# Optimization experiments

Hardware: AMD Instinct MI355X
Metric: run time of the kernel (lower is better)

## Reference

```python
import jax, jax.numpy as jnp
import numpy as np

B = 131072   # batch of states (e.g. ODE integrator batch)
S = 2        # state_dim (q, p)
H = 512      # hidden_dim
E = 8        # action_embedding_dim


def setup_inputs() -> dict:
    key = jax.random.key(0)
    ks = jax.random.split(key, 8)
    sc = lambda n: 1.0 / np.sqrt(n)
    return {
        "t": 0,  # unused time scalar (odeint signature)
        "state": jax.random.normal(ks[0], (B, S), dtype=jnp.float32),
        "action_emb": jax.random.normal(ks[1], (B, E), dtype=jnp.float32),
        # H_net: Linear(S,H) -> Softplus -> Linear(H,H) -> Softplus -> Linear(H,1)
        "W1": jax.random.normal(ks[2], (S, H), dtype=jnp.float32) * sc(S),
        "b1": jnp.zeros((H,), dtype=jnp.float32),
        "W2": jax.random.normal(ks[3], (H, H), dtype=jnp.float32) * sc(H),
        "b2": jnp.zeros((H,), dtype=jnp.float32),
        "W3": jax.random.normal(ks[4], (H, 1), dtype=jnp.float32) * sc(H),
        "b3": jnp.zeros((1,), dtype=jnp.float32),
        "log_damping": jnp.asarray(-1.0, dtype=jnp.float32),
        # G_net: Linear(E, S//2)
        "Gw": jax.random.normal(ks[5], (E, S // 2), dtype=jnp.float32) * sc(E),
        "Gb": jnp.zeros((S // 2,), dtype=jnp.float32),
    }


def reference(t, state, action_emb, W1, b1, W2, b2, W3, b3, log_damping, Gw, Gb):
    # Hamiltonian net: scalar H per state; sum over batch so jax.grad gives
    # per-sample dH/dstate in one pass (equivalent to autograd.grad with ones cotangent).
    def H_sum(s):
        h = jax.nn.softplus(s @ W1 + b1)       # [B, H]
        h = jax.nn.softplus(h @ W2 + b2)       # [B, H]
        return jnp.sum(h @ W3 + b3)            # scalar

    dH_dstate = jax.grad(H_sum)(state)         # [B, S]
    dH_dq = dH_dstate[..., 0:1]                # [B, 1]
    dH_dp = dH_dstate[..., 1:2]                # [B, 1]

    damping = jnp.exp(log_damping)
    G_u = action_emb @ Gw + Gb                 # [B, 1]

    dq_dt = dH_dp
    dp_dt = -dH_dq - damping * dH_dp + G_u
    return jnp.concatenate([dq_dt, dp_dt], axis=-1)  # [B, S]
```

## Files before the change

### kernel.cpp

```cpp
#include <hip/hip_runtime.h>

typedef __bf16 bf16x8 __attribute__((ext_vector_type(8)));
typedef float f32x4 __attribute__((ext_vector_type(4)));
typedef unsigned short u16x8 __attribute__((ext_vector_type(8)));

#define DEVI static __device__ __forceinline__

DEVI unsigned short f2b(float x) {
  __bf16 b = (__bf16)x;
  return __builtin_bit_cast(unsigned short, b);
}

__global__ __launch_bounds__(256) void pack_w2_kernel(
    const float* __restrict__ W2, unsigned short* __restrict__ p1,
    unsigned short* __restrict__ p2) {
  int idx = blockIdx.x * 256 + threadIdx.x;
  int which = idx >> 18;
  int i = idx & 262143;
  int j = i & 7;
  int l = (i >> 3) & 63;
  int t0 = (i >> 9) & 31;
  int t1 = i >> 14;
  if (which == 0) {
    p1[i] = f2b(W2[(t1 * 32 + (l >> 4) * 8 + j) * 512 + t0 * 16 + (l & 15)]);
  } else {
    p2[i] = f2b(W2[(t0 * 16 + (l & 15)) * 512 + t1 * 32 + (l >> 4) * 8 + j]);
  }
}

__global__ __launch_bounds__(256, 2) void phm_kernel(
    const float* __restrict__ state, const float* __restrict__ action_emb,
    const float* __restrict__ W1, const float* __restrict__ b1,
    const float* __restrict__ b2, const float* __restrict__ W3,
    const float* __restrict__ log_damping, const float* __restrict__ Gw,
    const float* __restrict__ Gb, const unsigned short* __restrict__ packB1,
    const unsigned short* __restrict__ packB2, float* __restrict__ out) {
  __shared__ unsigned short buf[64 * 512];
  __shared__ float W1s[1024];
  __shared__ float b1s[512];
  __shared__ float b2s[512];
  __shared__ float W3s[512];
  __shared__ float st[128];
  __shared__ float part[4][64][2];

  const int t = threadIdx.x;
  const int lane = t & 63;
  const int wid = t >> 6;
  const int l15 = lane & 15;
  const int l4 = lane >> 4;
  const long row0 = (long)blockIdx.x * 64;
  const f32x4 fzero = {0.f, 0.f, 0.f, 0.f};

  for (int i = t; i < 512; i += 256) {
    W1s[i] = W1[i];
    W1s[512 + i] = W1[512 + i];
    b1s[i] = b1[i];
    b2s[i] = b2[i];
    W3s[i] = W3[i];
  }
  if (t < 128) st[t] = state[row0 * 2 + t];
  __syncthreads();

  for (int it = 0; it < 16; ++it) {
    int gid = it * 256 + t;
    int r = gid >> 6;
    int cg = gid & 63;
    float s0 = st[r * 2], s1 = st[r * 2 + 1];
    u16x8 pk;
#pragma unroll
    for (int j = 0; j < 8; ++j) {
      int c = cg * 8 + j;
      float z = fmaf(s0, W1s[c], fmaf(s1, W1s[512 + c], b1s[c]));
      float e = __expf(-fabsf(z));
      float h = fmaxf(z, 0.f) + __logf(1.f + e);
      pk[j] = f2b(h);
    }
    int bo = (cg * 16) ^ ((r & 15) << 4);
    *reinterpret_cast<u16x8*>(reinterpret_cast<char*>(buf) + r * 1024 + bo) = pk;
  }
  __syncthreads();

  f32x4 acc1[2][4][4];
#pragma unroll
  for (int ch = 0; ch < 2; ++ch)
#pragma unroll
    for (int a = 0; a < 4; ++a)
#pragma unroll
      for (int b = 0; b < 4; ++b) acc1[ch][a][b] = fzero;

#pragma unroll
  for (int chunk = 0; chunk < 2; ++chunk) {
    const int c0 = wid * 128 + chunk * 64;
#pragma unroll 2
    for (int kt = 0; kt < 16; ++kt) {
      bf16x8 af[4];
      int bo = (kt * 64 + l4 * 16) ^ (l15 << 4);
#pragma unroll
      for (int rt = 0; rt < 4; ++rt) {
        int rr = rt * 16 + l15;
        af[rt] = __builtin_bit_cast(
            bf16x8, *reinterpret_cast<const int4*>(
                        reinterpret_cast<const char*>(buf) + rr * 1024 + bo));
      }
      bf16x8 bfr[4];
#pragma unroll
      for (int ct = 0; ct < 4; ++ct) {
        int frag = kt * 32 + (c0 >> 4) + ct;
        bfr[ct] = __builtin_bit_cast(
            bf16x8,
            *reinterpret_cast<const int4*>(packB1 + (frag * 64 + lane) * 8));
      }
#pragma unroll
      for (int rt = 0; rt < 4; ++rt)
#pragma unroll
        for (int ct = 0; ct < 4; ++ct)
          acc1[chunk][rt][ct] = __builtin_amdgcn_mfma_f32_16x16x32_bf16(
              af[rt], bfr[ct], acc1[chunk][rt][ct], 0, 0, 0);
    }
  }
  __syncthreads();

#pragma unroll
  for (int chunk = 0; chunk < 2; ++chunk) {
    const int c0 = wid * 128 + chunk * 64;
#pragma unroll
    for (int ct = 0; ct < 4; ++ct) {
      int c = c0 + ct * 16 + l15;
      float w3 = W3s[c], bb = b2s[c];
#pragma unroll
      for (int rt = 0; rt < 4; ++rt) {
#pragma unroll
        for (int j = 0; j < 4; ++j) {
          int r = rt * 16 + l4 * 4 + j;
          float z2 = acc1[chunk][rt][ct][j] + bb;
          float sg = __builtin_amdgcn_rcpf(1.f + __expf(-z2));
          unsigned short u = f2b(w3 * sg);
          int bo = (c * 2) ^ ((r & 15) << 4);
          *reinterpret_cast<unsigned short*>(
              reinterpret_cast<char*>(buf) + r * 1024 + bo) = u;
        }
      }
    }
  }
  __syncthreads();

  float2 sv[16];
#pragma unroll
  for (int rt = 0; rt < 4; ++rt)
#pragma unroll
    for (int j = 0; j < 4; ++j) {
      int r = rt * 16 + l4 * 4 + j;
      sv[rt * 4 + j] = *reinterpret_cast<const float2*>(&st[r * 2]);
    }

  float p0[16], p1v[16];
#pragma unroll
  for (int i = 0; i < 16; ++i) { p0[i] = 0.f; p1v[i] = 0.f; }

  for (int chunk = 0; chunk < 2; ++chunk) {
    const int k0c = wid * 128 + chunk * 64;
    f32x4 acc[4][4];
#pragma unroll
    for (int a = 0; a < 4; ++a)
#pragma unroll
      for (int b = 0; b < 4; ++b) acc[a][b] = fzero;

#pragma unroll 2
    for (int ct2 = 0; ct2 < 16; ++ct2) {
      bf16x8 af[4];
      int bo = (ct2 * 64 + l4 * 16) ^ (l15 << 4);
#pragma unroll
      for (int rt = 0; rt < 4; ++rt) {
        int rr = rt * 16 + l15;
        af[rt] = __builtin_bit_cast(
            bf16x8, *reinterpret_cast<const int4*>(
                        reinterpret_cast<const char*>(buf) + rr * 1024 + bo));
      }
      bf16x8 bfr[4];
#pragma unroll
      for (int kt = 0; kt < 4; ++kt) {
        int frag = ct2 * 32 + (k0c >> 4) + kt;
        bfr[kt] = __builtin_bit_cast(
            bf16x8,
            *reinterpret_cast<const int4*>(packB2 + (frag * 64 + lane) * 8));
      }
#pragma unroll
      for (int rt = 0; rt < 4; ++rt)
#pragma unroll
        for (int kt = 0; kt < 4; ++kt)
          acc[rt][kt] = __builtin_amdgcn_mfma_f32_16x16x32_bf16(
              af[rt], bfr[kt], acc[rt][kt], 0, 0, 0);
    }
#pragma unroll
    for (int kt = 0; kt < 4; ++kt) {
      int kc = k0c + kt * 16 + l15;
      float w10 = W1s[kc], w11 = W1s[512 + kc], bb = b1s[kc];
#pragma unroll
      for (int rt = 0; rt < 4; ++rt) {
#pragma unroll
        for (int j = 0; j < 4; ++j) {
          float2 s = sv[rt * 4 + j];
          float z1 = fmaf(s.x, w10, fmaf(s.y, w11, bb));
          float sg = __builtin_amdgcn_rcpf(1.f + __expf(-z1));
          float dz1 = acc[rt][kt][j] * sg;
          p0[rt * 4 + j] = fmaf(dz1, w10, p0[rt * 4 + j]);
          p1v[rt * 4 + j] = fmaf(dz1, w11, p1v[rt * 4 + j]);
        }
      }
    }
  }

#pragma unroll
  for (int i = 0; i < 16; ++i) {
    float a = p0[i], b = p1v[i];
    for (int m = 1; m < 16; m <<= 1) {
      a += __shfl_xor(a, m, 64);
      b += __shfl_xor(b, m, 64);
    }
    p0[i] = a;
    p1v[i] = b;
  }
  if (l15 == 0) {
#pragma unroll
    for (int rt = 0; rt < 4; ++rt)
#pragma unroll
      for (int j = 0; j < 4; ++j) {
        int r = rt * 16 + l4 * 4 + j;
        part[wid][r][0] = p0[rt * 4 + j];
        part[wid][r][1] = p1v[rt * 4 + j];
      }
  }
  __syncthreads();

  if (t < 64) {
    long grow = row0 + t;
    float g0 = part[0][t][0] + part[1][t][0] + part[2][t][0] + part[3][t][0];
    float g1 = part[0][t][1] + part[1][t][1] + part[2][t][1] + part[3][t][1];
    const float4 ae0 = reinterpret_cast<const float4*>(action_emb)[grow * 2];
    const float4 ae1 = reinterpret_cast<const float4*>(action_emb)[grow * 2 + 1];
    float gu = Gb[0];
    gu = fmaf(ae0.x, Gw[0], gu);
    gu = fmaf(ae0.y, Gw[1], gu);
    gu = fmaf(ae0.z, Gw[2], gu);
    gu = fmaf(ae0.w, Gw[3], gu);
    gu = fmaf(ae1.x, Gw[4], gu);
    gu = fmaf(ae1.y, Gw[5], gu);
    gu = fmaf(ae1.z, Gw[6], gu);
    gu = fmaf(ae1.w, Gw[7], gu);
    float damping = __expf(log_damping[0]);
    float2 o;
    o.x = g1;
    o.y = -g0 - damping * g1 + gu;
    reinterpret_cast<float2*>(out)[grow] = o;
  }
}

extern "C" void kernel_launch(void* const* d_in, const int* in_sizes, int n_in,
                              void* d_out, int out_size, void* d_ws,
                              size_t ws_size, hipStream_t stream) {
  const float* state = (const float*)d_in[1];
  const float* action_emb = (const float*)d_in[2];
  const float* W1 = (const float*)d_in[3];
  const float* b1 = (const float*)d_in[4];
  const float* W2 = (const float*)d_in[5];
  const float* b2 = (const float*)d_in[6];
  const float* W3 = (const float*)d_in[7];
  const float* log_damping = (const float*)d_in[9];
  const float* Gw = (const float*)d_in[10];
  const float* Gb = (const float*)d_in[11];
  float* out = (float*)d_out;

  unsigned short* p1 = (unsigned short*)d_ws;
  unsigned short* p2 = p1 + 262144;

  pack_w2_kernel<<<dim3(2048), dim3(256), 0, stream>>>(W2, p1, p2);
  phm_kernel<<<dim3(2048), dim3(256), 0, stream>>>(
      state, action_emb, W1, b1, b2, W3, log_damping, Gw, Gb, p1, p2, out);
}
```

Before: 177.5 us.

## Use 32x32x16 MFMA for forward GEMM with fragment-ordered LDS layout

Switches the forward H@W2 GEMM from 16x16x32 to 32x32x16 bf16 MFMA tiles, with a matching repacking of W2. The first hidden activations are stored in LDS as pre-swizzled, fragment-contiguous pages, so each lane reads its operand with one linear 16-byte load. The backward GEMM is restructured to keep all 8 column tiles of 16x16 accumulators live in a single pass instead of two chunks. The intent is fewer MFMA issues, simpler LDS addressing and fewer repeated A-fragment loads. The trade-off is higher register pressure and more complex scatter writes for the sigmoid-gradient stage.

```diff
diff --git a/kernel.cpp b/kernel.cpp
--- a/kernel.cpp
+++ b/kernel.cpp
@@ -2,6 +2,7 @@
 
 typedef __bf16 bf16x8 __attribute__((ext_vector_type(8)));
 typedef float f32x4 __attribute__((ext_vector_type(4)));
+typedef float f32x16 __attribute__((ext_vector_type(16)));
 typedef unsigned short u16x8 __attribute__((ext_vector_type(8)));
 
 #define DEVI static __device__ __forceinline__
@@ -19,12 +20,14 @@
   int i = idx & 262143;
   int j = i & 7;
   int l = (i >> 3) & 63;
-  int t0 = (i >> 9) & 31;
-  int t1 = i >> 14;
   if (which == 0) {
-    p1[i] = f2b(W2[(t1 * 32 + (l >> 4) * 8 + j) * 512 + t0 * 16 + (l & 15)]);
+    int t0 = (i >> 9) & 15;
+    int s = i >> 13;
+    p1[i] = f2b(W2[(s * 16 + (l >> 5) * 8 + j) * 512 + t0 * 32 + (l & 31)]);
   } else {
-    p2[i] = f2b(W2[(t0 * 16 + (l & 15)) * 512 + t1 * 32 + (l >> 4) * 8 + j]);
+    int t0 = (i >> 9) & 31;
+    int s = i >> 14;
+    p2[i] = f2b(W2[(t0 * 16 + (l & 15)) * 512 + s * 32 + (l >> 4) * 8 + j]);
   }
 }
 
@@ -48,8 +51,10 @@
   const int wid = t >> 6;
   const int l15 = lane & 15;
   const int l4 = lane >> 4;
+  const int l31 = lane & 31;
+  const int l5 = lane >> 5;
   const long row0 = (long)blockIdx.x * 64;
-  const f32x4 fzero = {0.f, 0.f, 0.f, 0.f};
+  char* bufc = reinterpret_cast<char*>(buf);
 
   for (int i = t; i < 512; i += 256) {
     W1s[i] = W1[i];
@@ -62,150 +67,136 @@
   __syncthreads();
 
   for (int it = 0; it < 16; ++it) {
-    int gid = it * 256 + t;
-    int r = gid >> 6;
-    int cg = gid & 63;
-    float s0 = st[r * 2], s1 = st[r * 2 + 1];
+    int page = it * 4 + wid;
+    int s = page >> 1, rt = page & 1;
+    int row = rt * 32 + l31;
+    int k0 = s * 16 + l5 * 8;
+    float s0 = st[row * 2], s1 = st[row * 2 + 1];
     u16x8 pk;
 #pragma unroll
     for (int j = 0; j < 8; ++j) {
-      int c = cg * 8 + j;
+      int c = k0 + j;
       float z = fmaf(s0, W1s[c], fmaf(s1, W1s[512 + c], b1s[c]));
       float e = __expf(-fabsf(z));
       float h = fmaxf(z, 0.f) + __logf(1.f + e);
       pk[j] = f2b(h);
     }
-    int bo = (cg * 16) ^ ((r & 15) << 4);
-    *reinterpret_cast<u16x8*>(reinterpret_cast<char*>(buf) + r * 1024 + bo) = pk;
-  }
-  __syncthreads();
-
-  f32x4 acc1[2][4][4];
-#pragma unroll
-  for (int ch = 0; ch < 2; ++ch)
-#pragma unroll
-    for (int a = 0; a < 4; ++a)
-#pragma unroll
-      for (int b = 0; b < 4; ++b) acc1[ch][a][b] = fzero;
-
-#pragma unroll
-  for (int chunk = 0; chunk < 2; ++chunk) {
-    const int c0 = wid * 128 + chunk * 64;
+    *reinterpret_cast<u16x8*>(bufc + page * 1024 + lane * 16) = pk;
+  }
+  __syncthreads();
+
+  f32x16 acc1[2][4];
+#pragma unroll
+  for (int rt = 0; rt < 2; ++rt)
+#pragma unroll
+    for (int ct = 0; ct < 4; ++ct)
+#pragma unroll
+      for (int r = 0; r < 16; ++r) acc1[rt][ct][r] = 0.f;
+
+#pragma unroll 4
+  for (int s = 0; s < 32; ++s) {
+    bf16x8 af[2];
+#pragma unroll
+    for (int rt = 0; rt < 2; ++rt)
+      af[rt] = __builtin_bit_cast(
+          bf16x8, *reinterpret_cast<const int4*>(
+                      bufc + (s * 2 + rt) * 1024 + lane * 16));
+    bf16x8 bfr[4];
+#pragma unroll
+    for (int ct = 0; ct < 4; ++ct)
+      bfr[ct] = __builtin_bit_cast(
+          bf16x8, *reinterpret_cast<const int4*>(
+                      packB1 + ((s * 16 + wid * 4 + ct) * 64 + lane) * 8));
+#pragma unroll
+    for (int rt = 0; rt < 2; ++rt)
+#pragma unroll
+      for (int ct = 0; ct < 4; ++ct)
+        acc1[rt][ct] = __builtin_amdgcn_mfma_f32_32x32x16_bf16(
+            af[rt], bfr[ct], acc1[rt][ct], 0, 0, 0);
+  }
+  __syncthreads();
+
+#pragma unroll
+  for (int rt = 0; rt < 2; ++rt) {
+#pragma unroll
+    for (int ct = 0; ct < 4; ++ct) {
+      int c = wid * 128 + ct * 32 + l31;
+      float w3 = W3s[c], bb = b2s[c];
+      int pbase = (c >> 5) * 4096 + (c & 7) * 2;
+      int oct = (l31 >> 3);
+#pragma unroll
+      for (int reg = 0; reg < 16; ++reg) {
+        int row = rt * 32 + (reg & 3) + 8 * (reg >> 2) + 4 * l5;
+        float z2 = acc1[rt][ct][reg] + bb;
+        float sg = __builtin_amdgcn_rcpf(1.f + __expf(-z2));
+        unsigned short u = f2b(w3 * sg);
+        int lane2 = (row & 15) + 16 * oct;
+        int slot = lane2 ^ (lane2 >> 4);
+        *reinterpret_cast<unsigned short*>(
+            bufc + pbase + (row >> 4) * 1024 + slot * 16) = u;
+      }
+    }
+  }
+  __syncthreads();
+
+  float2 sv[16];
+#pragma unroll
+  for (int rt2 = 0; rt2 < 4; ++rt2)
+#pragma unroll
+    for (int jj = 0; jj < 4; ++jj) {
+      int r = rt2 * 16 + l4 * 4 + jj;
+      sv[rt2 * 4 + jj] = *reinterpret_cast<const float2*>(&st[r * 2]);
+    }
+
+  f32x4 acc2[4][8];
+#pragma unroll
+  for (int a = 0; a < 4; ++a)
+#pragma unroll
+    for (int b = 0; b < 8; ++b)
+#pragma unroll
+      for (int r = 0; r < 4; ++r) acc2[a][b][r] = 0.f;
+
+  const int rslot = (lane ^ (lane >> 4)) * 16;
 #pragma unroll 2
-    for (int kt = 0; kt < 16; ++kt) {
-      bf16x8 af[4];
-      int bo = (kt * 64 + l4 * 16) ^ (l15 << 4);
-#pragma unroll
-      for (int rt = 0; rt < 4; ++rt) {
-        int rr = rt * 16 + l15;
-        af[rt] = __builtin_bit_cast(
-            bf16x8, *reinterpret_cast<const int4*>(
-                        reinterpret_cast<const char*>(buf) + rr * 1024 + bo));
-      }
-      bf16x8 bfr[4];
-#pragma unroll
-      for (int ct = 0; ct < 4; ++ct) {
-        int frag = kt * 32 + (c0 >> 4) + ct;
-        bfr[ct] = __builtin_bit_cast(
-            bf16x8,
-            *reinterpret_cast<const int4*>(packB1 + (frag * 64 + lane) * 8));
-      }
-#pragma unroll
-      for (int rt = 0; rt < 4; ++rt)
-#pragma unroll
-        for (int ct = 0; ct < 4; ++ct)
-          acc1[chunk][rt][ct] = __builtin_amdgcn_mfma_f32_16x16x32_bf16(
-              af[rt], bfr[ct], acc1[chunk][rt][ct], 0, 0, 0);
-    }
-  }
-  __syncthreads();
-
-#pragma unroll
-  for (int chunk = 0; chunk < 2; ++chunk) {
-    const int c0 = wid * 128 + chunk * 64;
-#pragma unroll
-    for (int ct = 0; ct < 4; ++ct) {
-      int c = c0 + ct * 16 + l15;
-      float w3 = W3s[c], bb = b2s[c];
-#pragma unroll
-      for (int rt = 0; rt < 4; ++rt) {
-#pragma unroll
-        for (int j = 0; j < 4; ++j) {
-          int r = rt * 16 + l4 * 4 + j;
-          float z2 = acc1[chunk][rt][ct][j] + bb;
-          float sg = __builtin_amdgcn_rcpf(1.f + __expf(-z2));
-          unsigned short u = f2b(w3 * sg);
-          int bo = (c * 2) ^ ((r & 15) << 4);
-          *reinterpret_cast<unsigned short*>(
-              reinterpret_cast<char*>(buf) + r * 1024 + bo) = u;
-        }
-      }
-    }
-  }
-  __syncthreads();
-
-  float2 sv[16];
-#pragma unroll
-  for (int rt = 0; rt < 4; ++rt)
-#pragma unroll
-    for (int j = 0; j < 4; ++j) {
-      int r = rt * 16 + l4 * 4 + j;
-      sv[rt * 4 + j] = *reinterpret_cast<const float2*>(&st[r * 2]);
-    }
+  for (int s2 = 0; s2 < 16; ++s2) {
+    bf16x8 af[4];
+#pragma unroll
+    for (int rt2 = 0; rt2 < 4; ++rt2)
+      af[rt2] = __builtin_bit_cast(
+          bf16x8, *reinterpret_cast<const int4*>(
+                      bufc + s2 * 4096 + rt2 * 1024 + rslot));
+    bf16x8 bfr[8];
+#pragma unroll
+    for (int ct2 = 0; ct2 < 8; ++ct2)
+      bfr[ct2] = __builtin_bit_cast(
+          bf16x8, *reinterpret_cast<const int4*>(
+                      packB2 + ((s2 * 32 + wid * 8 + ct2) * 64 + lane) * 8));
+#pragma unroll
+    for (int rt2 = 0; rt2 < 4; ++rt2)
+#pragma unroll
+      for (int ct2 = 0; ct2 < 8; ++ct2)
+        acc2[rt2][ct2] = __builtin_amdgcn_mfma_f32_16x16x32_bf16(
+            af[rt2], bfr[ct2], acc2[rt2][ct2], 0, 0, 0);
+  }
 
   float p0[16], p1v[16];
 #pragma unroll
   for (int i = 0; i < 16; ++i) { p0[i] = 0.f; p1v[i] = 0.f; }
 
-  for (int chunk = 0; chunk < 2; ++chunk) {
-    const int k0c = wid * 128 + chunk * 64;
-    f32x4 acc[4][4];
-#pragma unroll
-    for (int a = 0; a < 4; ++a)
-#pragma unroll
-      for (int b = 0; b < 4; ++b) acc[a][b] = fzero;
-
-#pragma unroll 2
-    for (int ct2 = 0; ct2 < 16; ++ct2) {
-      bf16x8 af[4];
-      int bo = (ct2 * 64 + l4 * 16) ^ (l15 << 4);
-#pragma unroll
-      for (int rt = 0; rt < 4; ++rt) {
-        int rr = rt * 16 + l15;
-        af[rt] = __builtin_bit_cast(
-            bf16x8, *reinterpret_cast<const int4*>(
-                        reinterpret_cast<const char*>(buf) + rr * 1024 + bo));
-      }
-      bf16x8 bfr[4];
-#pragma unroll
-      for (int kt = 0; kt < 4; ++kt) {
-        int frag = ct2 * 32 + (k0c >> 4) + kt;
-        bfr[kt] = __builtin_bit_cast(
-            bf16x8,
-            *reinterpret_cast<const int4*>(packB2 + (frag * 64 + lane) * 8));
-      }
-#pragma unroll
-      for (int rt = 0; rt < 4; ++rt)
-#pragma unroll
-        for (int kt = 0; kt < 4; ++kt)
-          acc[rt][kt] = __builtin_amdgcn_mfma_f32_16x16x32_bf16(
-              af[rt], bfr[kt], acc[rt][kt], 0, 0, 0);
-    }
-#pragma unroll
-    for (int kt = 0; kt < 4; ++kt) {
-      int kc = k0c + kt * 16 + l15;
-      float w10 = W1s[kc], w11 = W1s[512 + kc], bb = b1s[kc];
-#pragma unroll
-      for (int rt = 0; rt < 4; ++rt) {
-#pragma unroll
-        for (int j = 0; j < 4; ++j) {
-          float2 s = sv[rt * 4 + j];
-          float z1 = fmaf(s.x, w10, fmaf(s.y, w11, bb));
-          float sg = __builtin_amdgcn_rcpf(1.f + __expf(-z1));
-          float dz1 = acc[rt][kt][j] * sg;
-          p0[rt * 4 + j] = fmaf(dz1, w10, p0[rt * 4 + j]);
-          p1v[rt * 4 + j] = fmaf(dz1, w11, p1v[rt * 4 + j]);
-        }
+#pragma unroll
+  for (int ct2 = 0; ct2 < 8; ++ct2) {
+    int hc = wid * 128 + ct2 * 16 + l15;
+    float w10 = W1s[hc], w11 = W1s[512 + hc], bb = b1s[hc];
+#pragma unroll
+    for (int rt2 = 0; rt2 < 4; ++rt2) {
+#pragma unroll
+      for (int jj = 0; jj < 4; ++jj) {
+        float2 sp = sv[rt2 * 4 + jj];
+        float z1 = fmaf(sp.x, w10, fmaf(sp.y, w11, bb));
+        float sg = __builtin_amdgcn_rcpf(1.f + __expf(-z1));
+        float dz1 = acc2[rt2][ct2][jj] * sg;
+        p0[rt2 * 4 + jj] = fmaf(dz1, w10, p0[rt2 * 4 + jj]);
+        p1v[rt2 * 4 + jj] = fmaf(dz1, w11, p1v[rt2 * 4 + jj]);
       }
     }
   }
@@ -222,12 +213,12 @@
   }
   if (l15 == 0) {
 #pragma unroll
-    for (int rt = 0; rt < 4; ++rt)
-#pragma unroll
-      for (int j = 0; j < 4; ++j) {
-        int r = rt * 16 + l4 * 4 + j;
-        part[wid][r][0] = p0[rt * 4 + j];
-        part[wid][r][1] = p1v[rt * 4 + j];
+    for (int rt2 = 0; rt2 < 4; ++rt2)
+#pragma unroll
+      for (int jj = 0; jj < 4; ++jj) {
+        int r = rt2 * 16 + l4 * 4 + jj;
+        part[wid][r][0] = p0[rt2 * 4 + jj];
+        part[wid][r][1] = p1v[rt2 * 4 + jj];
       }
   }
   __syncthreads();
```

Result: no change. 177.6 us (+0.1%).
